# Kernel tuning notes

Measured on AMD Instinct MI355X. Metric: run time of the kernel, lower is better.

Reference implementation:

```python
import jax, jax.numpy as jnp
import numpy as np

B, H_IN, H_OUT, SEQ_LEN = 256, 512, 512, 512


def setup_inputs() -> dict:
    key = jax.random.key(0)
    k1, k2, k3, k4, k5 = jax.random.split(key, 5)
    s = 1.0 / np.sqrt(H_OUT)  # torch GRU init scale
    return {
        "x": jax.random.normal(k1, (B, H_IN), dtype=jnp.float32),
        "W_ih": jax.random.uniform(k2, (3 * H_OUT, H_IN), jnp.float32, -s, s),
        "W_hh": jax.random.uniform(k3, (3 * H_OUT, H_OUT), jnp.float32, -s, s),
        "b_ih": jax.random.uniform(k4, (3 * H_OUT,), jnp.float32, -s, s),
        "b_hh": jax.random.uniform(k5, (3 * H_OUT,), jnp.float32, -s, s),
        "seq_len": SEQ_LEN,
    }


def reference(x, W_ih, W_hh, b_ih, b_hh, seq_len):
    # bridge: ReLU, then the same vector is fed at every timestep, so the
    # input-to-hidden projection is computed ONCE and reused across the scan.
    xr = jax.nn.relu(x)                       # [B, H_in]
    gi = xr @ W_ih.T + b_ih                   # [B, 3*H_out], constant over time
    Hh = W_hh.shape[1]
    gi_r, gi_z, gi_n = gi[:, :Hh], gi[:, Hh:2 * Hh], gi[:, 2 * Hh:]

    h0 = jnp.zeros((x.shape[0], Hh), dtype=x.dtype)

    def step(h, _):
        gh = h @ W_hh.T + b_hh                # [B, 3*H_out]
        gh_r, gh_z, gh_n = gh[:, :Hh], gh[:, Hh:2 * Hh], gh[:, 2 * Hh:]
        r = jax.nn.sigmoid(gi_r + gh_r)
        z = jax.nn.sigmoid(gi_z + gh_z)
        n = jnp.tanh(gi_n + r * gh_n)
        h_new = (1.0 - z) * n + z * h
        return h_new, h_new

    _, hs = jax.lax.scan(step, h0, None, length=seq_len)  # [S, B, H_out]
    return jnp.transpose(hs, (1, 0, 2))                   # [B, S, H_out]
```

## Files before the change

### kernel.cpp

```cpp
#include <hip/hip_runtime.h>


typedef __attribute__((ext_vector_type(8))) short short8;
typedef __attribute__((ext_vector_type(4))) float f32x4;
typedef unsigned short ushort_t;
typedef unsigned int uint_t;
typedef unsigned long long u64_t;

#define NG 16
#define NM 16
#define NB 16
#define NJ 32
#define TPB 384
#define SPIN_MAX (1u << 16)
#define ABORT_IDX 8192
#define GBUF_BASE 16384
#define GRP_U32 8192
#define BUF_U32 131072

__device__ __forceinline__ ushort_t bf16_rne(float f) {
  uint_t u = __float_as_uint(f);
  return (ushort_t)((u + 0x7fffu + ((u >> 16) & 1u)) >> 16);
}
__device__ __forceinline__ float bf16f(ushort_t h) {
  return __uint_as_float(((uint_t)h) << 16);
}
__device__ __forceinline__ int gRow(int rs, int m) {
  int base = m * NJ;
  if (rs < 32) return base + rs;
  if (rs < 64) return 512 + base + (rs - 32);
  return 1024 + base + (rs - 64);
}

template <bool LO>
__device__ __forceinline__ void loadW(short8* dst, const float* __restrict__ W,
                                      int tile, int m, int lane) {
  int rs = tile * 16 + (lane & 15);
  const float* p = W + (size_t)gRow(rs, m) * 512 + ((lane >> 4) << 3);
#pragma unroll
  for (int c = 0; c < 16; ++c) {
    const float* pc = p + c * 32;
    short8 o;
#pragma unroll
    for (int i = 0; i < 8; ++i) {
      float v = pc[i];
      ushort_t hi = bf16_rne(v);
      o[i] = LO ? (short)bf16_rne(v - bf16f(hi)) : (short)hi;
    }
    dst[c] = o;
  }
}

__global__ __launch_bounds__(TPB, 1) void gru_kernel(
    const float* __restrict__ x, const float* __restrict__ Wih,
    const float* __restrict__ Whh, const float* __restrict__ bih,
    const float* __restrict__ bhh, float* __restrict__ out,
    uint_t* __restrict__ wsp, int NT) {
  __shared__ __align__(16) char s_hhi[NB * 1024];
  __shared__ __align__(16) char s_hlo[NB * 1024];
  __shared__ float s_gi[96 * 17];
  __shared__ float s_gh[96 * 17];
  __shared__ float s_hloc[NB * NJ];
  __shared__ float s_bhh[NJ];
  __shared__ int s_stop;

  const int tid = threadIdx.x;
  const int lane = tid & 63;
  const int w = tid >> 6;
  const int bid = blockIdx.x;
  const int g = bid & 15;
  const int m = bid >> 4;
  if (NT <= 0) return;

  uint_t* flags = wsp;
  uint_t* gbuf = wsp + GBUF_BASE;

  for (int i = tid; i < NB * 64; i += TPB) {
    int b = i >> 6, k0 = (i & 63) << 3;
    const float* px = x + (size_t)(g * NB + b) * 512 + k0;
    short8 vh, vl;
#pragma unroll
    for (int ii = 0; ii < 8; ++ii) {
      float xv = px[ii];
      xv = xv > 0.f ? xv : 0.f;
      ushort_t hb = bf16_rne(xv);
      vh[ii] = (short)hb;
      vl[ii] = (short)bf16_rne(xv - bf16f(hb));
    }
    int off = ((b << 10) + (k0 << 1)) ^ ((b & 7) << 4);
    *(short8*)(s_hhi + off) = vh;
    *(short8*)(s_hlo + off) = vl;
  }
  if (tid < NJ) s_bhh[tid] = bhh[1024 + m * NJ + tid];
  if (tid == 0) s_stop = 0;
  __syncthreads();

  short8 wA[16], wB[16];
  const f32x4 vzero = {0.f, 0.f, 0.f, 0.f};
  f32x4 acc0 = vzero, acc1 = vzero;
  const int bcol = lane & 15;
  const int swzb = (bcol & 7) << 4;
  const int kb0 = (lane >> 4) << 4;

  if (w < 3) {
    loadW<false>(wA, Wih, 2 * w, m, lane);
    loadW<false>(wB, Wih, 2 * w + 1, m, lane);
#pragma unroll
    for (int c = 0; c < 16; ++c) {
      int off = ((bcol << 10) + (c << 6) + kb0) ^ swzb;
      short8 bh = *(const short8*)(s_hhi + off);
      short8 bl = *(const short8*)(s_hlo + off);
      acc0 = __builtin_amdgcn_mfma_f32_16x16x32_bf16(wA[c], bh, acc0, 0, 0, 0);
      acc0 = __builtin_amdgcn_mfma_f32_16x16x32_bf16(wA[c], bl, acc0, 0, 0, 0);
      acc1 = __builtin_amdgcn_mfma_f32_16x16x32_bf16(wB[c], bh, acc1, 0, 0, 0);
      acc1 = __builtin_amdgcn_mfma_f32_16x16x32_bf16(wB[c], bl, acc1, 0, 0, 0);
    }
    loadW<true>(wA, Wih, 2 * w, m, lane);
    loadW<true>(wB, Wih, 2 * w + 1, m, lane);
#pragma unroll
    for (int c = 0; c < 16; ++c) {
      int off = ((bcol << 10) + (c << 6) + kb0) ^ swzb;
      short8 bh = *(const short8*)(s_hhi + off);
      acc0 = __builtin_amdgcn_mfma_f32_16x16x32_bf16(wA[c], bh, acc0, 0, 0, 0);
      acc1 = __builtin_amdgcn_mfma_f32_16x16x32_bf16(wB[c], bh, acc1, 0, 0, 0);
    }
  }
  __syncthreads();
  if (w < 3) {
    int drow = (lane >> 4) << 2;
#pragma unroll
    for (int q = 0; q < 4; ++q) {
      int rs0 = 2 * w * 16 + drow + q, rs1 = rs0 + 16;
      int g0 = gRow(rs0, m), g1 = gRow(rs1, m);
      s_gi[rs0 * 17 + bcol] = acc0[q] + bih[g0] + (rs0 < 64 ? bhh[g0] : 0.f);
      s_gi[rs1 * 17 + bcol] = acc1[q] + bih[g1] + (rs1 < 64 ? bhh[g1] : 0.f);
    }
    loadW<false>(wA, Whh, 2 * w, m, lane);
    loadW<false>(wB, Whh, 2 * w + 1, m, lane);
  }
  for (int i = tid; i < 4096; i += TPB) {
    ((int*)s_hhi)[i] = 0;
    ((int*)s_hlo)[i] = 0;
  }
  for (int i = tid; i < NB * NJ; i += TPB) s_hloc[i] = 0.f;
  __syncthreads();

  const size_t outRow = (size_t)NT * 512;
  float* outBase = out + (size_t)(g * NB) * outRow + m * NJ;

  for (int t = 0; t < NT; ++t) {
    if (w < 3) {
      acc0 = vzero;
      acc1 = vzero;
#pragma unroll
      for (int c = 0; c < 16; ++c) {
        int off = ((bcol << 10) + (c << 6) + kb0) ^ swzb;
        short8 bh = *(const short8*)(s_hhi + off);
        short8 bl = *(const short8*)(s_hlo + off);
        acc0 = __builtin_amdgcn_mfma_f32_16x16x32_bf16(wA[c], bh, acc0, 0, 0, 0);
        acc0 = __builtin_amdgcn_mfma_f32_16x16x32_bf16(wA[c], bl, acc0, 0, 0, 0);
        acc1 = __builtin_amdgcn_mfma_f32_16x16x32_bf16(wB[c], bh, acc1, 0, 0, 0);
        acc1 = __builtin_amdgcn_mfma_f32_16x16x32_bf16(wB[c], bl, acc1, 0, 0, 0);
      }
      int drow = (lane >> 4) << 2;
#pragma unroll
      for (int q = 0; q < 4; ++q) {
        s_gh[(2 * w * 16 + drow + q) * 17 + bcol] = acc0[q];
        s_gh[((2 * w + 1) * 16 + drow + q) * 17 + bcol] = acc1[q];
      }
    }
    __syncthreads();

    u64_t* dstq = (u64_t*)(gbuf + (size_t)(t & 1) * BUF_U32 + g * GRP_U32 +
                           m * 512);
    if (tid < 256) {
      int b = tid >> 4, j0 = (tid & 15) << 1;
      float hn01[2];
#pragma unroll
      for (int e = 0; e < 2; ++e) {
        int j = j0 + e;
        float pr = s_gi[j * 17 + b] + s_gh[j * 17 + b];
        float pz = s_gi[(32 + j) * 17 + b] + s_gh[(32 + j) * 17 + b];
        float r = 1.f / (1.f + __expf(-pr));
        float z = 1.f / (1.f + __expf(-pz));
        float pn =
            s_gi[(64 + j) * 17 + b] + r * (s_gh[(64 + j) * 17 + b] + s_bhh[j]);
        float n = 1.f - 2.f / (1.f + __expf(2.f * pn));
        float hn = n + z * (s_hloc[b * 32 + j] - n);
        s_hloc[b * 32 + j] = hn;
        hn01[e] = hn;
      }
      float2 ov = {hn01[0], hn01[1]};
      *(float2*)(outBase + (size_t)b * outRow + (size_t)t * 512 + j0) = ov;
      ushort_t h0 = bf16_rne(hn01[0]);
      ushort_t h1 = bf16_rne(hn01[1]);
      uint_t p0 = (uint_t)h0 | ((uint_t)bf16_rne(hn01[0] - bf16f(h0)) << 16);
      uint_t p1 = (uint_t)h1 | ((uint_t)bf16_rne(hn01[1] - bf16f(h1)) << 16);
      u64_t pq = (u64_t)p0 | ((u64_t)p1 << 32);
      __hip_atomic_store(dstq + tid, pq, __ATOMIC_RELAXED,
                         __HIP_MEMORY_SCOPE_AGENT);
    }
    __syncthreads();

    if (tid == 0)
      __hip_atomic_store(&flags[((g << 4) + m) << 5], (uint_t)(t + 1),
                         __ATOMIC_RELAXED, __HIP_MEMORY_SCOPE_AGENT);
    if (w == 0) {
      const uint_t tgt = (uint_t)(t + 1);
      uint_t* fp = flags + (((g << 4) + (lane & 15)) << 5);
      uint_t sp = 0;
      for (;;) {
        uint_t v = 0xffffffffu;
        if (lane < 16)
          v = __hip_atomic_load(fp, __ATOMIC_RELAXED, __HIP_MEMORY_SCOPE_AGENT);
        if (__all((int)(v >= tgt))) break;
        ++sp;
        uint_t ab = 0;
        if ((sp & 127u) == 0u) {
          ab = __hip_atomic_load(&flags[ABORT_IDX], __ATOMIC_RELAXED,
                                 __HIP_MEMORY_SCOPE_AGENT);
          if (sp > SPIN_MAX) {
            __hip_atomic_store(&flags[ABORT_IDX], 1u, __ATOMIC_RELAXED,
                               __HIP_MEMORY_SCOPE_AGENT);
            ab = 1;
          }
        }
        if (__any((int)(ab != 0))) {
          if (tid == 0) s_stop = 1;
          break;
        }
        __builtin_amdgcn_s_sleep(1);
      }
    }
    __syncthreads();
    if (s_stop) break;

    {
      const u64_t* srcq =
          (const u64_t*)(gbuf + (size_t)(t & 1) * BUF_U32 + g * GRP_U32);
#define LDI(k)                                                                 \
  __hip_atomic_load(srcq + (tid + (k) * TPB), __ATOMIC_RELAXED,                \
                    __HIP_MEMORY_SCOPE_AGENT)
      u64_t q0 = LDI(0), q1 = LDI(1), q2 = LDI(2), q3 = LDI(3), q4 = LDI(4);
      u64_t q5 = LDI(5), q6 = LDI(6), q7 = LDI(7), q8 = LDI(8), q9 = LDI(9);
      u64_t q10 = (tid < 256) ? LDI(10) : 0ull;
#undef LDI
#define UNP(k, qq)                                                             \
  {                                                                            \
    int i = tid + (k) * TPB;                                                   \
    int mcol = ((i >> 8) << 5) + ((i & 15) << 1);                              \
    int b = (i >> 4) & 15;                                                     \
    int off = ((b << 10) + (mcol << 1)) ^ ((b & 7) << 4);                      \
    uint_t w0 = (uint_t)(qq), w1 = (uint_t)((qq) >> 32);                       \
    *(uint_t*)(s_hhi + off) = (w0 & 0xffffu) | ((w1 & 0xffffu) << 16);         \
    *(uint_t*)(s_hlo + off) = (w0 >> 16) | (w1 & 0xffff0000u);                 \
  }
      UNP(0, q0) UNP(1, q1) UNP(2, q2) UNP(3, q3) UNP(4, q4) UNP(5, q5)
      UNP(6, q6) UNP(7, q7) UNP(8, q8) UNP(9, q9)
      if (tid < 256) UNP(10, q10)
#undef UNP
    }
    __syncthreads();
  }
}

extern "C" void kernel_launch(void* const* d_in, const int* in_sizes, int n_in,
                              void* d_out, int out_size, void* d_ws,
                              size_t ws_size, hipStream_t stream) {
  const float* x = (const float*)d_in[0];
  const float* Wih = (const float*)d_in[1];
  const float* Whh = (const float*)d_in[2];
  const float* bih = (const float*)d_in[3];
  const float* bhh = (const float*)d_in[4];
  float* out = (float*)d_out;
  int NT = out_size / (256 * 512);
  uint_t* wsp = (uint_t*)d_ws;
  hipMemsetAsync(d_ws, 0, 65536, stream);
  hipLaunchKernelGGL(gru_kernel, dim3(NG * NM), dim3(TPB), 0, stream, x, Wih,
                     Whh, bih, bhh, out, wsp, NT);
}
```

Before: 1.408 ms.

## Feed MFMA B-operands straight from global exchange buffer, drop LDS unpack stage

The recurrent matvec now loads the hi/lo bf16 hidden-state fragments directly from the global double buffer in MFMA operand layout, instead of first copying them into swizzled LDS and syncing. The writer side stores separate hi and lo planes laid out to match, and the accumulators are split so hi and lo products form independent MFMA chains. Gate threads move to waves 1-4 so wave 5 can spin on flags while the output stores are issued non-temporally, and the last step skips its wait. This removes one barrier and the LDS round trip per timestep, at the cost of every compute wave reading global/L2 memory on the critical path, plus a larger workspace memset.

```diff
diff --git a/kernel.cpp b/kernel.cpp
--- a/kernel.cpp
+++ b/kernel.cpp
@@ -3,6 +3,7 @@
 
 typedef __attribute__((ext_vector_type(8))) short short8;
 typedef __attribute__((ext_vector_type(4))) float f32x4;
+typedef __attribute__((ext_vector_type(2))) float f32x2;
 typedef unsigned short ushort_t;
 typedef unsigned int uint_t;
 typedef unsigned long long u64_t;
@@ -18,12 +19,23 @@
 #define GRP_U32 8192
 #define BUF_U32 131072
 
+#define ALD(P) __hip_atomic_load((P), __ATOMIC_RELAXED, __HIP_MEMORY_SCOPE_AGENT)
+
 __device__ __forceinline__ ushort_t bf16_rne(float f) {
   uint_t u = __float_as_uint(f);
   return (ushort_t)((u + 0x7fffu + ((u >> 16) & 1u)) >> 16);
 }
 __device__ __forceinline__ float bf16f(ushort_t h) {
   return __uint_as_float(((uint_t)h) << 16);
+}
+__device__ __forceinline__ short8 mk8(u64_t a, u64_t b) {
+  union {
+    u64_t q[2];
+    short8 s;
+  } u;
+  u.q[0] = a;
+  u.q[1] = b;
+  return u.s;
 }
 __device__ __forceinline__ int gRow(int rs, int m) {
   int base = m * NJ;
@@ -138,10 +150,6 @@
     loadW<false>(wA, Whh, 2 * w, m, lane);
     loadW<false>(wB, Whh, 2 * w + 1, m, lane);
   }
-  for (int i = tid; i < 4096; i += TPB) {
-    ((int*)s_hhi)[i] = 0;
-    ((int*)s_hlo)[i] = 0;
-  }
   for (int i = tid; i < NB * NJ; i += TPB) s_hloc[i] = 0.f;
   __syncthreads();
 
@@ -150,35 +158,41 @@
 
   for (int t = 0; t < NT; ++t) {
     if (w < 3) {
-      acc0 = vzero;
-      acc1 = vzero;
-#pragma unroll
-      for (int c = 0; c < 16; ++c) {
-        int off = ((bcol << 10) + (c << 6) + kb0) ^ swzb;
-        short8 bh = *(const short8*)(s_hhi + off);
-        short8 bl = *(const short8*)(s_hlo + off);
-        acc0 = __builtin_amdgcn_mfma_f32_16x16x32_bf16(wA[c], bh, acc0, 0, 0, 0);
-        acc0 = __builtin_amdgcn_mfma_f32_16x16x32_bf16(wA[c], bl, acc0, 0, 0, 0);
-        acc1 = __builtin_amdgcn_mfma_f32_16x16x32_bf16(wB[c], bh, acc1, 0, 0, 0);
-        acc1 = __builtin_amdgcn_mfma_f32_16x16x32_bf16(wB[c], bl, acc1, 0, 0, 0);
-      }
+      const u64_t* sq = (const u64_t*)gbuf + (size_t)(t & 1) * (BUF_U32 / 2) +
+                        g * (GRP_U32 / 2);
+      const int lofs = (bcol << 3) + ((lane >> 4) << 1);
+      f32x4 a0h = vzero, a0l = vzero, a1h = vzero, a1l = vzero;
+#pragma unroll
+      for (int p = 0; p < 16; ++p) {
+        const u64_t* pp = sq + p * 256 + lofs;
+        u64_t h0 = ALD(pp);
+        u64_t h1 = ALD(pp + 1);
+        u64_t l0 = ALD(pp + 128);
+        u64_t l1 = ALD(pp + 129);
+        short8 bh = mk8(h0, h1), bl = mk8(l0, l1);
+        a0h = __builtin_amdgcn_mfma_f32_16x16x32_bf16(wA[p], bh, a0h, 0, 0, 0);
+        a1h = __builtin_amdgcn_mfma_f32_16x16x32_bf16(wB[p], bh, a1h, 0, 0, 0);
+        a0l = __builtin_amdgcn_mfma_f32_16x16x32_bf16(wA[p], bl, a0l, 0, 0, 0);
+        a1l = __builtin_amdgcn_mfma_f32_16x16x32_bf16(wB[p], bl, a1l, 0, 0, 0);
+      }
+      f32x4 r0 = a0h + a0l, r1 = a1h + a1l;
       int drow = (lane >> 4) << 2;
 #pragma unroll
       for (int q = 0; q < 4; ++q) {
-        s_gh[(2 * w * 16 + drow + q) * 17 + bcol] = acc0[q];
-        s_gh[((2 * w + 1) * 16 + drow + q) * 17 + bcol] = acc1[q];
+        s_gh[(2 * w * 16 + drow + q) * 17 + bcol] = r0[q];
+        s_gh[((2 * w + 1) * 16 + drow + q) * 17 + bcol] = r1[q];
       }
     }
     __syncthreads();
 
-    u64_t* dstq = (u64_t*)(gbuf + (size_t)(t & 1) * BUF_U32 + g * GRP_U32 +
-                           m * 512);
-    if (tid < 256) {
-      int b = tid >> 4, j0 = (tid & 15) << 1;
-      float hn01[2];
-#pragma unroll
-      for (int e = 0; e < 2; ++e) {
-        int j = j0 + e;
+    const int gt = tid - 64;
+    float hn0 = 0.f, hn1 = 0.f;
+    uint_t* eb =
+        gbuf + (size_t)((t & 1) ^ 1) * BUF_U32 + g * GRP_U32 + m * 512;
+    if ((unsigned)gt < 256u) {
+      int b = gt >> 4, j0 = (gt & 15) << 1;
+      {
+        int j = j0;
         float pr = s_gi[j * 17 + b] + s_gh[j * 17 + b];
         float pz = s_gi[(32 + j) * 17 + b] + s_gh[(32 + j) * 17 + b];
         float r = 1.f / (1.f + __expf(-pr));
@@ -186,39 +200,53 @@
         float pn =
             s_gi[(64 + j) * 17 + b] + r * (s_gh[(64 + j) * 17 + b] + s_bhh[j]);
         float n = 1.f - 2.f / (1.f + __expf(2.f * pn));
-        float hn = n + z * (s_hloc[b * 32 + j] - n);
-        s_hloc[b * 32 + j] = hn;
-        hn01[e] = hn;
-      }
-      float2 ov = {hn01[0], hn01[1]};
-      *(float2*)(outBase + (size_t)b * outRow + (size_t)t * 512 + j0) = ov;
-      ushort_t h0 = bf16_rne(hn01[0]);
-      ushort_t h1 = bf16_rne(hn01[1]);
-      uint_t p0 = (uint_t)h0 | ((uint_t)bf16_rne(hn01[0] - bf16f(h0)) << 16);
-      uint_t p1 = (uint_t)h1 | ((uint_t)bf16_rne(hn01[1] - bf16f(h1)) << 16);
-      u64_t pq = (u64_t)p0 | ((u64_t)p1 << 32);
-      __hip_atomic_store(dstq + tid, pq, __ATOMIC_RELAXED,
+        hn0 = n + z * (s_hloc[b * 32 + j] - n);
+        s_hloc[b * 32 + j] = hn0;
+      }
+      {
+        int j = j0 + 1;
+        float pr = s_gi[j * 17 + b] + s_gh[j * 17 + b];
+        float pz = s_gi[(32 + j) * 17 + b] + s_gh[(32 + j) * 17 + b];
+        float r = 1.f / (1.f + __expf(-pr));
+        float z = 1.f / (1.f + __expf(-pz));
+        float pn =
+            s_gi[(64 + j) * 17 + b] + r * (s_gh[(64 + j) * 17 + b] + s_bhh[j]);
+        float n = 1.f - 2.f / (1.f + __expf(2.f * pn));
+        hn1 = n + z * (s_hloc[b * 32 + j] - n);
+        s_hloc[b * 32 + j] = hn1;
+      }
+      ushort_t hA = bf16_rne(hn0), hB = bf16_rne(hn1);
+      uint_t phi = (uint_t)hA | ((uint_t)hB << 16);
+      uint_t plo = (uint_t)bf16_rne(hn0 - bf16f(hA)) |
+                   ((uint_t)bf16_rne(hn1 - bf16f(hB)) << 16);
+      __hip_atomic_store(eb + gt, phi, __ATOMIC_RELAXED,
                          __HIP_MEMORY_SCOPE_AGENT);
+      __hip_atomic_store(eb + 256 + gt, plo, __ATOMIC_RELAXED,
+                         __HIP_MEMORY_SCOPE_AGENT);
     }
     __syncthreads();
 
-    if (tid == 0)
+    if (tid == 256)
       __hip_atomic_store(&flags[((g << 4) + m) << 5], (uint_t)(t + 1),
                          __ATOMIC_RELAXED, __HIP_MEMORY_SCOPE_AGENT);
-    if (w == 0) {
+    if ((unsigned)gt < 256u) {
+      int b = gt >> 4, j0 = (gt & 15) << 1;
+      f32x2 ov = {hn0, hn1};
+      __builtin_nontemporal_store(
+          ov, (f32x2*)(outBase + (size_t)b * outRow + (size_t)t * 512 + j0));
+    }
+    if (w == 5 && t + 1 < NT) {
       const uint_t tgt = (uint_t)(t + 1);
       uint_t* fp = flags + (((g << 4) + (lane & 15)) << 5);
       uint_t sp = 0;
       for (;;) {
         uint_t v = 0xffffffffu;
-        if (lane < 16)
-          v = __hip_atomic_load(fp, __ATOMIC_RELAXED, __HIP_MEMORY_SCOPE_AGENT);
+        if (lane < 16) v = ALD(fp);
         if (__all((int)(v >= tgt))) break;
         ++sp;
         uint_t ab = 0;
         if ((sp & 127u) == 0u) {
-          ab = __hip_atomic_load(&flags[ABORT_IDX], __ATOMIC_RELAXED,
-                                 __HIP_MEMORY_SCOPE_AGENT);
+          ab = ALD(&flags[ABORT_IDX]);
           if (sp > SPIN_MAX) {
             __hip_atomic_store(&flags[ABORT_IDX], 1u, __ATOMIC_RELAXED,
                                __HIP_MEMORY_SCOPE_AGENT);
@@ -226,7 +254,7 @@
           }
         }
         if (__any((int)(ab != 0))) {
-          if (tid == 0) s_stop = 1;
+          if (lane == 0) s_stop = 1;
           break;
         }
         __builtin_amdgcn_s_sleep(1);
@@ -234,33 +262,6 @@
     }
     __syncthreads();
     if (s_stop) break;
-
-    {
-      const u64_t* srcq =
-          (const u64_t*)(gbuf + (size_t)(t & 1) * BUF_U32 + g * GRP_U32);
-#define LDI(k)                                                                 \
-  __hip_atomic_load(srcq + (tid + (k) * TPB), __ATOMIC_RELAXED,                \
-                    __HIP_MEMORY_SCOPE_AGENT)
-      u64_t q0 = LDI(0), q1 = LDI(1), q2 = LDI(2), q3 = LDI(3), q4 = LDI(4);
-      u64_t q5 = LDI(5), q6 = LDI(6), q7 = LDI(7), q8 = LDI(8), q9 = LDI(9);
-      u64_t q10 = (tid < 256) ? LDI(10) : 0ull;
-#undef LDI
-#define UNP(k, qq)                                                             \
-  {                                                                            \
-    int i = tid + (k) * TPB;                                                   \
-    int mcol = ((i >> 8) << 5) + ((i & 15) << 1);                              \
-    int b = (i >> 4) & 15;                                                     \
-    int off = ((b << 10) + (mcol << 1)) ^ ((b & 7) << 4);                      \
-    uint_t w0 = (uint_t)(qq), w1 = (uint_t)((qq) >> 32);                       \
-    *(uint_t*)(s_hhi + off) = (w0 & 0xffffu) | ((w1 & 0xffffu) << 16);         \
-    *(uint_t*)(s_hlo + off) = (w0 >> 16) | (w1 & 0xffff0000u);                 \
-  }
-      UNP(0, q0) UNP(1, q1) UNP(2, q2) UNP(3, q3) UNP(4, q4) UNP(5, q5)
-      UNP(6, q6) UNP(7, q7) UNP(8, q8) UNP(9, q9)
-      if (tid < 256) UNP(10, q10)
-#undef UNP
-    }
-    __syncthreads();
   }
 }
 
@@ -275,7 +276,7 @@
   float* out = (float*)d_out;
   int NT = out_size / (256 * 512);
   uint_t* wsp = (uint_t*)d_ws;
-  hipMemsetAsync(d_ws, 0, 65536, stream);
+  (void)hipMemsetAsync(d_ws, 0, 65536 + BUF_U32 * 4, stream);
   hipLaunchKernelGGL(gru_kernel, dim3(NG * NM), dim3(TPB), 0, stream, x, Wih,
                      Whh, bih, bhh, out, wsp, NT);
 }
```

Result: slower. 2.643 ms (+87.7%).
